# Optimization experiments

Hardware: AMD Instinct MI355X
Metric: run time of the kernel (lower is better)

The kernel has to match this reference:

```python
import jax, jax.numpy as jnp
import numpy as np


def _nn_mean_sqdist(source, target):
    # source: [N,3], target: [M,3]
    s_norm = jnp.sum(source ** 2, axis=1, keepdims=True)          # [N,1]
    t_norm = jnp.sum(target ** 2, axis=1, keepdims=True)          # [M,1]
    dist = s_norm + t_norm.T - 2.0 * (source @ target.T)          # [N,M] squared dists
    return jnp.min(dist, axis=1).mean()


def setup_inputs() -> dict:
    key = jax.random.key(0)
    k1, k2 = jax.random.split(key)
    pred_positions = jax.random.normal(k1, (16384, 3), dtype=jnp.float32)
    target_positions = jax.random.normal(k2, (16384, 3), dtype=jnp.float32)
    return {"pred_positions": pred_positions, "target_positions": target_positions}


def reference(pred_positions, target_positions):
    d_pt = _nn_mean_sqdist(pred_positions, target_positions)
    d_tp = _nn_mean_sqdist(target_positions, pred_positions)  # use_bidirectional=True
    return (d_pt + d_tp) / 2.0
```

## Files before the change

### kernel.cpp

```cpp
#include <hip/hip_runtime.h>

#define TPB 256

typedef __attribute__((ext_vector_type(8))) short bf16x8;
typedef __attribute__((ext_vector_type(16))) float f32x16;

__device__ inline unsigned short f2bf(float f) {
    unsigned u = __float_as_uint(f);
    return (unsigned short)((u + 0x7FFFu + ((u >> 16) & 1u)) >> 16);
}
__device__ inline float bf2f(unsigned short h) {
    return __uint_as_float((unsigned)h << 16);
}
__device__ inline uint4 pack8(unsigned short s0, unsigned short s1,
                              unsigned short s2, unsigned short s3,
                              unsigned short s4, unsigned short s5,
                              unsigned short s6, unsigned short s7) {
    uint4 v;
    v.x = (unsigned)s0 | ((unsigned)s1 << 16);
    v.y = (unsigned)s2 | ((unsigned)s3 << 16);
    v.z = (unsigned)s4 | ((unsigned)s5 << 16);
    v.w = (unsigned)s6 | ((unsigned)s7 << 16);
    return v;
}
__device__ inline bf16x8 as_frag(uint4 v) {
    union { uint4 u; bf16x8 f; } c; c.u = v; return c.f;
}

__global__ __launch_bounds__(TPB) void prep_kernel(
        const float* __restrict__ a, const float* __restrict__ b,
        uint4* __restrict__ pAa, uint4* __restrict__ pBa,
        uint4* __restrict__ pAb, uint4* __restrict__ pBb,
        float* __restrict__ norms, unsigned* __restrict__ pmins,
        float* __restrict__ acc, unsigned* __restrict__ cnt, int n) {
    int idx = blockIdx.x * TPB + threadIdx.x;
    if (idx < 2 * n) {
        int isB = idx >= n;
        int i = isB ? idx - n : idx;
        const float* s = isB ? b : a;
        float x = s[3 * i], y = s[3 * i + 1], z = s[3 * i + 2];
        float w = x * x + y * y + z * z;
        norms[idx] = w;
        float ax = -2.0f * x, ay = -2.0f * y, az = -2.0f * z;
        unsigned short ahx = f2bf(ax), ahy = f2bf(ay), ahz = f2bf(az);
        unsigned short alx = f2bf(ax - bf2f(ahx));
        unsigned short aly = f2bf(ay - bf2f(ahy));
        unsigned short alz = f2bf(az - bf2f(ahz));
        unsigned short thx = f2bf(x), thy = f2bf(y), thz = f2bf(z);
        unsigned short tlx = f2bf(x - bf2f(thx));
        unsigned short tly = f2bf(y - bf2f(thy));
        unsigned short tlz = f2bf(z - bf2f(thz));
        unsigned short wh = f2bf(w);  float r1 = w - bf2f(wh);
        unsigned short wm = f2bf(r1); float r2 = r1 - bf2f(wm);
        unsigned short wl = f2bf(r2);
        const unsigned short ONE = 0x3F80;
        uint4* Ad = (isB ? pAb : pAa) + (size_t)i * 2;
        uint4* Bd = (isB ? pBb : pBa) + (size_t)i * 2;
        Ad[0] = pack8(ahx, ahy, ahz, alx, aly, alz, ahx, ahy);
        Ad[1] = pack8(ahz, ONE, ONE, ONE, alx, aly, alz, 0);
        Bd[0] = pack8(thx, thy, thz, thx, thy, thz, tlx, tly);
        Bd[1] = pack8(tlz, wh, wm, wl, tlx, tly, tlz, 0);
        pmins[idx] = 0xFFFFFFFFu;
    }
    if (idx == 0) { acc[0] = 0.0f; cnt[0] = 0u; }
}

#define COMPUTE_TILE(X) do {                                                   \
    bf16x8 bb = as_frag(X);                                                    \
    f32x16 d0 = __builtin_amdgcn_mfma_f32_32x32x16_bf16(a0, bb, z, 0, 0, 0);   \
    f32x16 d1 = __builtin_amdgcn_mfma_f32_32x32x16_bf16(a1, bb, z, 0, 0, 0);   \
    _Pragma("unroll")                                                          \
    for (int i = 0; i < 16; ++i) {                                             \
        rm0[i] = fminf(rm0[i], d0[i]);                                         \
        rm1[i] = fminf(rm1[i], d1[i]);                                         \
    }                                                                          \
} while (0)

__global__ __launch_bounds__(TPB, 4) void minpass_kernel(
        const uint4* __restrict__ pAa, const uint4* __restrict__ pBa,
        const uint4* __restrict__ pAb, const uint4* __restrict__ pBb,
        const float* __restrict__ norms, unsigned* __restrict__ pmins, int n) {
    const int TS = 8;
    const int NRB = n / 256;
    const int TGT = n / TS;
    const int NT = TGT / 32;

    int bid = blockIdx.x;
    int dir = bid / (NRB * TS);
    int rem = bid % (NRB * TS);
    int rbk = rem / TS;
    int ts  = rem % TS;

    const uint4* __restrict__ Ap = dir ? pAb : pAa;
    const uint4* __restrict__ Bp = dir ? pBa : pBb;

    const int tid = threadIdx.x;
    const int wid = tid >> 6, lane = tid & 63;
    const int lr = lane & 31, lh = lane >> 5;

    const int rowbase = rbk * 256 + wid * 64;
    bf16x8 a0 = as_frag(Ap[(size_t)(rowbase + lr) * 2 + lh]);
    bf16x8 a1 = as_frag(Ap[(size_t)(rowbase + 32 + lr) * 2 + lh]);

    float rm0[16], rm1[16];
#pragma unroll
    for (int i = 0; i < 16; ++i) { rm0[i] = __builtin_inff(); rm1[i] = __builtin_inff(); }
    f32x16 z = {};

    const uint4* __restrict__ bp = Bp + (size_t)(ts * TGT + lr) * 2 + lh;

    uint4 A0 = bp[0], A1 = bp[64], A2 = bp[128], A3 = bp[192];
    for (int t = 0; t < NT - 4; t += 4) {
        COMPUTE_TILE(A0); A0 = bp[(t + 4) * 64];
        COMPUTE_TILE(A1); A1 = bp[(t + 5) * 64];
        COMPUTE_TILE(A2); A2 = bp[(t + 6) * 64];
        COMPUTE_TILE(A3); A3 = bp[(t + 7) * 64];
    }
    COMPUTE_TILE(A0); COMPUTE_TILE(A1); COMPUTE_TILE(A2); COMPUTE_TILE(A3);

#pragma unroll
    for (int k = 1; k < 32; k <<= 1) {
#pragma unroll
        for (int i = 0; i < 16; ++i) {
            rm0[i] = fminf(rm0[i], __shfl_xor(rm0[i], k, 64));
            rm1[i] = fminf(rm1[i], __shfl_xor(rm1[i], k, 64));
        }
    }
    if (lr == 0) {
        unsigned* pm = pmins + (size_t)dir * n;
        const float* nb = norms + (dir ? n : 0);
        int rb0 = rowbase + lh * 4;
#pragma unroll
        for (int i = 0; i < 16; ++i) {
            int r = (i & 3) + ((i >> 2) << 3);
            int r0 = rb0 + r, r1 = rb0 + 32 + r;
            atomicMin(&pm[r0], __float_as_uint(rm0[i] + nb[r0]));
            atomicMin(&pm[r1], __float_as_uint(rm1[i] + nb[r1]));
        }
    }
}

__global__ __launch_bounds__(TPB) void finalize_kernel(
        const uint4* __restrict__ pmins, float* __restrict__ acc,
        unsigned* __restrict__ cnt, float* __restrict__ out, int n, int nblocks) {
    int i = blockIdx.x * TPB + threadIdx.x;
    uint4 v = pmins[i];
    float sum = __uint_as_float(v.x) + __uint_as_float(v.y)
              + __uint_as_float(v.z) + __uint_as_float(v.w);
    for (int off = 32; off > 0; off >>= 1)
        sum += __shfl_down(sum, off, 64);
    __shared__ float wsum[TPB / 64];
    int lane = threadIdx.x & 63, wid = threadIdx.x >> 6;
    if (lane == 0) wsum[wid] = sum;
    __syncthreads();
    if (threadIdx.x == 0) {
        float t = 0.0f;
        for (int w = 0; w < TPB / 64; ++w) t += wsum[w];
        atomicAdd(acc, t);
        __threadfence();
        unsigned old = atomicAdd(cnt, 1u);
        if (old == (unsigned)(nblocks - 1)) {
            float a0 = atomicAdd(acc, 0.0f);
            out[0] = a0 / (float)(2 * n);
        }
    }
}

extern "C" void kernel_launch(void* const* d_in, const int* in_sizes, int n_in,
                              void* d_out, int out_size, void* d_ws, size_t ws_size,
                              hipStream_t stream) {
    const float* a = (const float*)d_in[0];
    const float* b = (const float*)d_in[1];
    int n = in_sizes[0] / 3;
    float* out = (float*)d_out;
    char* ws = (char*)d_ws;
    float* acc = (float*)ws;
    unsigned* cnt = (unsigned*)(ws + 8);
    float* norms = (float*)(ws + 256);
    char* packs = ws + 256 + (size_t)2 * n * 4;
    size_t psz = (size_t)n * 32;
    uint4* pAa = (uint4*)(packs);
    uint4* pBa = (uint4*)(packs + psz);
    uint4* pAb = (uint4*)(packs + 2 * psz);
    uint4* pBb = (uint4*)(packs + 3 * psz);
    unsigned* pmins = (unsigned*)(packs + 4 * psz);

    prep_kernel<<<(2 * n + TPB - 1) / TPB, TPB, 0, stream>>>(
        a, b, pAa, pBa, pAb, pBb, norms, pmins, acc, cnt, n);
    int mblocks = 2 * (n / 256) * 8;
    minpass_kernel<<<mblocks, TPB, 0, stream>>>(
        pAa, pBa, pAb, pBb, norms, pmins, n);
    int fblocks = (2 * n / 4) / TPB;
    finalize_kernel<<<fblocks, TPB, 0, stream>>>(
        (const uint4*)pmins, acc, cnt, out, n, fblocks);
}
```

Before: 85.64 us.

## Stage target tile in LDS and double the target split count

Each block now cooperatively copies its slice of packed target fragments into shared memory, then streams MFMA B operands from LDS instead of from global memory with register prefetch. The target dimension split goes from 8 to 16, so each block handles 1024 targets and the grid doubles. The aim is to cut the global/L2 load latency in the inner loop and add parallelism. The cost is more blocks, twice as many atomicMin writes, a 33KB LDS footprint that may limit occupancy, and a read one tile past the end into the padded buffer.

After: 93.87 us. 1.1x slower.

```diff
diff --git a/kernel.cpp b/kernel.cpp
--- a/kernel.cpp
+++ b/kernel.cpp
@@ -65,22 +65,11 @@
     if (idx == 0) { acc[0] = 0.0f; cnt[0] = 0u; }
 }
 
-#define COMPUTE_TILE(X) do {                                                   \
-    bf16x8 bb = as_frag(X);                                                    \
-    f32x16 d0 = __builtin_amdgcn_mfma_f32_32x32x16_bf16(a0, bb, z, 0, 0, 0);   \
-    f32x16 d1 = __builtin_amdgcn_mfma_f32_32x32x16_bf16(a1, bb, z, 0, 0, 0);   \
-    _Pragma("unroll")                                                          \
-    for (int i = 0; i < 16; ++i) {                                             \
-        rm0[i] = fminf(rm0[i], d0[i]);                                         \
-        rm1[i] = fminf(rm1[i], d1[i]);                                         \
-    }                                                                          \
-} while (0)
-
 __global__ __launch_bounds__(TPB, 4) void minpass_kernel(
         const uint4* __restrict__ pAa, const uint4* __restrict__ pBa,
         const uint4* __restrict__ pAb, const uint4* __restrict__ pBb,
         const float* __restrict__ norms, unsigned* __restrict__ pmins, int n) {
-    const int TS = 8;
+    const int TS = 16;
     const int NRB = n / 256;
     const int TGT = n / TS;
     const int NT = TGT / 32;
@@ -94,10 +83,19 @@
     const uint4* __restrict__ Ap = dir ? pAb : pAa;
     const uint4* __restrict__ Bp = dir ? pBa : pBb;
 
+    __shared__ uint4 sbuf[2048 + 64];
+
     const int tid = threadIdx.x;
     const int wid = tid >> 6, lane = tid & 63;
     const int lr = lane & 31, lh = lane >> 5;
 
+    {
+        const uint4* __restrict__ gs = Bp + (size_t)ts * TGT * 2;
+#pragma unroll
+        for (int i = 0; i < 8; ++i)
+            sbuf[tid + i * TPB] = gs[tid + i * TPB];
+    }
+
     const int rowbase = rbk * 256 + wid * 64;
     bf16x8 a0 = as_frag(Ap[(size_t)(rowbase + lr) * 2 + lh]);
     bf16x8 a1 = as_frag(Ap[(size_t)(rowbase + 32 + lr) * 2 + lh]);
@@ -107,16 +105,34 @@
     for (int i = 0; i < 16; ++i) { rm0[i] = __builtin_inff(); rm1[i] = __builtin_inff(); }
     f32x16 z = {};
 
-    const uint4* __restrict__ bp = Bp + (size_t)(ts * TGT + lr) * 2 + lh;
-
-    uint4 A0 = bp[0], A1 = bp[64], A2 = bp[128], A3 = bp[192];
-    for (int t = 0; t < NT - 4; t += 4) {
-        COMPUTE_TILE(A0); A0 = bp[(t + 4) * 64];
-        COMPUTE_TILE(A1); A1 = bp[(t + 5) * 64];
-        COMPUTE_TILE(A2); A2 = bp[(t + 6) * 64];
-        COMPUTE_TILE(A3); A3 = bp[(t + 7) * 64];
-    }
-    COMPUTE_TILE(A0); COMPUTE_TILE(A1); COMPUTE_TILE(A2); COMPUTE_TILE(A3);
+    __syncthreads();
+
+    const uint4* __restrict__ sb = sbuf + ((lr << 1) | lh);
+
+    bf16x8 b0 = as_frag(sb[0]);
+    for (int t = 0; t < NT; t += 2) {
+        bf16x8 b1 = as_frag(sb[(t + 1) * 64]);
+        {
+            f32x16 d0 = __builtin_amdgcn_mfma_f32_32x32x16_bf16(a0, b0, z, 0, 0, 0);
+            f32x16 d1 = __builtin_amdgcn_mfma_f32_32x32x16_bf16(a1, b0, z, 0, 0, 0);
+#pragma unroll
+            for (int i = 0; i < 16; ++i) {
+                rm0[i] = fminf(rm0[i], d0[i]);
+                rm1[i] = fminf(rm1[i], d1[i]);
+            }
+        }
+        bf16x8 b2 = as_frag(sb[(t + 2) * 64]);
+        {
+            f32x16 d0 = __builtin_amdgcn_mfma_f32_32x32x16_bf16(a0, b1, z, 0, 0, 0);
+            f32x16 d1 = __builtin_amdgcn_mfma_f32_32x32x16_bf16(a1, b1, z, 0, 0, 0);
+#pragma unroll
+            for (int i = 0; i < 16; ++i) {
+                rm0[i] = fminf(rm0[i], d0[i]);
+                rm1[i] = fminf(rm1[i], d1[i]);
+            }
+        }
+        b0 = b2;
+    }
 
 #pragma unroll
     for (int k = 1; k < 32; k <<= 1) {
@@ -187,7 +203,7 @@
 
     prep_kernel<<<(2 * n + TPB - 1) / TPB, TPB, 0, stream>>>(
         a, b, pAa, pBa, pAb, pBb, norms, pmins, acc, cnt, n);
-    int mblocks = 2 * (n / 256) * 8;
+    int mblocks = 2 * (n / 256) * 16;
     minpass_kernel<<<mblocks, TPB, 0, stream>>>(
         pAa, pBa, pAb, pBb, norms, pmins, n);
     int fblocks = (2 * n / 4) / TPB;
```

## Compute both directions from one distance matrix using row and column minima

Applied to the files above, without the earlier changes.

Instead of computing the N×M distance matrix twice (once per direction), the kernel computes the full squared distance (both norms folded into the MFMA operands) once and takes row minima via registers/atomics and column minima via LDS atomicMin per tile. Per-block column minima are written to a workspace and reduced across 64 row blocks in the finalize kernel. This halves the MFMA work but adds per-tile column reductions, LDS atomics, a large intermediate buffer and lowers occupancy to 2 blocks per SIMD group.

Result: no change. 85.58 us (-0.1%).

```diff
diff --git a/kernel.cpp b/kernel.cpp
--- a/kernel.cpp
+++ b/kernel.cpp
@@ -29,23 +29,29 @@
 
 __global__ __launch_bounds__(TPB) void prep_kernel(
         const float* __restrict__ a, const float* __restrict__ b,
-        uint4* __restrict__ pAa, uint4* __restrict__ pBa,
-        uint4* __restrict__ pAb, uint4* __restrict__ pBb,
-        float* __restrict__ norms, unsigned* __restrict__ pmins,
+        uint4* __restrict__ pA, uint4* __restrict__ pB,
+        unsigned* __restrict__ pmins,
         float* __restrict__ acc, unsigned* __restrict__ cnt, int n) {
     int idx = blockIdx.x * TPB + threadIdx.x;
-    if (idx < 2 * n) {
-        int isB = idx >= n;
-        int i = isB ? idx - n : idx;
-        const float* s = isB ? b : a;
-        float x = s[3 * i], y = s[3 * i + 1], z = s[3 * i + 2];
+    const unsigned short ONE = 0x3F80;
+    if (idx < n) {
+        float x = a[3 * idx], y = a[3 * idx + 1], z = a[3 * idx + 2];
         float w = x * x + y * y + z * z;
-        norms[idx] = w;
         float ax = -2.0f * x, ay = -2.0f * y, az = -2.0f * z;
         unsigned short ahx = f2bf(ax), ahy = f2bf(ay), ahz = f2bf(az);
         unsigned short alx = f2bf(ax - bf2f(ahx));
         unsigned short aly = f2bf(ay - bf2f(ahy));
         unsigned short alz = f2bf(az - bf2f(ahz));
+        unsigned short wh = f2bf(w);  float r1 = w - bf2f(wh);
+        unsigned short wm = f2bf(r1); float r2 = r1 - bf2f(wm);
+        unsigned short wl = f2bf(r2);
+        pA[(size_t)idx * 2 + 0] = pack8(ahx, ahy, ahz, alx, aly, alz, ahx, ahy);
+        pA[(size_t)idx * 2 + 1] = pack8(ahz, wh, wm, wl, ONE, ONE, ONE, 0);
+        pmins[idx] = 0xFFFFFFFFu;
+    } else if (idx < 2 * n) {
+        int i = idx - n;
+        float x = b[3 * i], y = b[3 * i + 1], z = b[3 * i + 2];
+        float w = x * x + y * y + z * z;
         unsigned short thx = f2bf(x), thy = f2bf(y), thz = f2bf(z);
         unsigned short tlx = f2bf(x - bf2f(thx));
         unsigned short tly = f2bf(y - bf2f(thy));
@@ -53,19 +59,46 @@
         unsigned short wh = f2bf(w);  float r1 = w - bf2f(wh);
         unsigned short wm = f2bf(r1); float r2 = r1 - bf2f(wm);
         unsigned short wl = f2bf(r2);
-        const unsigned short ONE = 0x3F80;
-        uint4* Ad = (isB ? pAb : pAa) + (size_t)i * 2;
-        uint4* Bd = (isB ? pBb : pBa) + (size_t)i * 2;
-        Ad[0] = pack8(ahx, ahy, ahz, alx, aly, alz, ahx, ahy);
-        Ad[1] = pack8(ahz, ONE, ONE, ONE, alx, aly, alz, 0);
-        Bd[0] = pack8(thx, thy, thz, thx, thy, thz, tlx, tly);
-        Bd[1] = pack8(tlz, wh, wm, wl, tlx, tly, tlz, 0);
-        pmins[idx] = 0xFFFFFFFFu;
+        pB[(size_t)i * 2 + 0] = pack8(thx, thy, thz, thx, thy, thz, tlx, tly);
+        pB[(size_t)i * 2 + 1] = pack8(tlz, ONE, ONE, ONE, wh, wm, wl, 0);
     }
     if (idx == 0) { acc[0] = 0.0f; cnt[0] = 0u; }
 }
 
-#define COMPUTE_TILE(X) do {                                                   \
+__global__ __launch_bounds__(TPB, 2) void minpass_kernel(
+        const uint4* __restrict__ pA, const uint4* __restrict__ pB,
+        unsigned* __restrict__ pmins, unsigned* __restrict__ cm_out, int n) {
+    const int TS = 8;
+    const int NRB = n / 256;
+    const int TGT = n / TS;
+    const int NT = TGT / 32;
+
+    int bid = blockIdx.x;
+    int rbk = bid % NRB;
+    int ts  = bid / NRB;
+
+    __shared__ unsigned cm[2048];
+
+    const int tid = threadIdx.x;
+    for (int i = tid; i < TGT; i += TPB) cm[i] = 0xFFFFFFFFu;
+
+    const int wid = tid >> 6, lane = tid & 63;
+    const int lr = lane & 31, lh = lane >> 5;
+
+    const int rowbase = rbk * 256 + wid * 64;
+    bf16x8 a0 = as_frag(pA[(size_t)(rowbase + lr) * 2 + lh]);
+    bf16x8 a1 = as_frag(pA[(size_t)(rowbase + 32 + lr) * 2 + lh]);
+
+    float rm0[16], rm1[16];
+#pragma unroll
+    for (int i = 0; i < 16; ++i) { rm0[i] = __builtin_inff(); rm1[i] = __builtin_inff(); }
+    f32x16 z = {};
+
+    const uint4* __restrict__ bp = pB + (size_t)(ts * TGT + lr) * 2 + lh;
+
+    __syncthreads();
+
+#define TILE(X, T) do {                                                        \
     bf16x8 bb = as_frag(X);                                                    \
     f32x16 d0 = __builtin_amdgcn_mfma_f32_32x32x16_bf16(a0, bb, z, 0, 0, 0);   \
     f32x16 d1 = __builtin_amdgcn_mfma_f32_32x32x16_bf16(a1, bb, z, 0, 0, 0);   \
@@ -74,49 +107,27 @@
         rm0[i] = fminf(rm0[i], d0[i]);                                         \
         rm1[i] = fminf(rm1[i], d1[i]);                                         \
     }                                                                          \
+    float t8[8];                                                               \
+    _Pragma("unroll")                                                          \
+    for (int i = 0; i < 8; ++i)                                                \
+        t8[i] = fminf(fminf(d0[i], d0[i + 8]), fminf(d1[i], d1[i + 8]));       \
+    float c0 = fminf(fminf(t8[0], t8[1]), t8[2]);                              \
+    float c1 = fminf(fminf(t8[3], t8[4]), t8[5]);                              \
+    float c2 = fminf(t8[6], t8[7]);                                            \
+    float cmin = fminf(fminf(c0, c1), c2);                                     \
+    atomicMin(&cm[(T) * 32 + lr], __float_as_uint(cmin));                      \
 } while (0)
 
-__global__ __launch_bounds__(TPB, 4) void minpass_kernel(
-        const uint4* __restrict__ pAa, const uint4* __restrict__ pBa,
-        const uint4* __restrict__ pAb, const uint4* __restrict__ pBb,
-        const float* __restrict__ norms, unsigned* __restrict__ pmins, int n) {
-    const int TS = 8;
-    const int NRB = n / 256;
-    const int TGT = n / TS;
-    const int NT = TGT / 32;
-
-    int bid = blockIdx.x;
-    int dir = bid / (NRB * TS);
-    int rem = bid % (NRB * TS);
-    int rbk = rem / TS;
-    int ts  = rem % TS;
-
-    const uint4* __restrict__ Ap = dir ? pAb : pAa;
-    const uint4* __restrict__ Bp = dir ? pBa : pBb;
-
-    const int tid = threadIdx.x;
-    const int wid = tid >> 6, lane = tid & 63;
-    const int lr = lane & 31, lh = lane >> 5;
-
-    const int rowbase = rbk * 256 + wid * 64;
-    bf16x8 a0 = as_frag(Ap[(size_t)(rowbase + lr) * 2 + lh]);
-    bf16x8 a1 = as_frag(Ap[(size_t)(rowbase + 32 + lr) * 2 + lh]);
-
-    float rm0[16], rm1[16];
-#pragma unroll
-    for (int i = 0; i < 16; ++i) { rm0[i] = __builtin_inff(); rm1[i] = __builtin_inff(); }
-    f32x16 z = {};
-
-    const uint4* __restrict__ bp = Bp + (size_t)(ts * TGT + lr) * 2 + lh;
-
-    uint4 A0 = bp[0], A1 = bp[64], A2 = bp[128], A3 = bp[192];
-    for (int t = 0; t < NT - 4; t += 4) {
-        COMPUTE_TILE(A0); A0 = bp[(t + 4) * 64];
-        COMPUTE_TILE(A1); A1 = bp[(t + 5) * 64];
-        COMPUTE_TILE(A2); A2 = bp[(t + 6) * 64];
-        COMPUTE_TILE(A3); A3 = bp[(t + 7) * 64];
-    }
-    COMPUTE_TILE(A0); COMPUTE_TILE(A1); COMPUTE_TILE(A2); COMPUTE_TILE(A3);
+    uint4 P0 = bp[0], P1 = bp[64], P2 = bp[128], P3 = bp[192];
+    int t = 0;
+    for (; t + 4 < NT; t += 4) {
+        TILE(P0, t);     P0 = bp[(t + 4) * 64];
+        TILE(P1, t + 1); P1 = bp[(t + 5) * 64];
+        TILE(P2, t + 2); P2 = bp[(t + 6) * 64];
+        TILE(P3, t + 3); P3 = bp[(t + 7) * 64];
+    }
+    TILE(P0, t); TILE(P1, t + 1); TILE(P2, t + 2); TILE(P3, t + 3);
+#undef TILE
 
 #pragma unroll
     for (int k = 1; k < 32; k <<= 1) {
@@ -127,26 +138,45 @@
         }
     }
     if (lr == 0) {
-        unsigned* pm = pmins + (size_t)dir * n;
-        const float* nb = norms + (dir ? n : 0);
         int rb0 = rowbase + lh * 4;
 #pragma unroll
         for (int i = 0; i < 16; ++i) {
             int r = (i & 3) + ((i >> 2) << 3);
-            int r0 = rb0 + r, r1 = rb0 + 32 + r;
-            atomicMin(&pm[r0], __float_as_uint(rm0[i] + nb[r0]));
-            atomicMin(&pm[r1], __float_as_uint(rm1[i] + nb[r1]));
-        }
+            atomicMin(&pmins[rb0 + r], __float_as_uint(rm0[i]));
+            atomicMin(&pmins[rb0 + 32 + r], __float_as_uint(rm1[i]));
+        }
+    }
+
+    __syncthreads();
+    {
+        unsigned* __restrict__ co = cm_out + (size_t)rbk * n + ts * TGT;
+        for (int i = tid; i < TGT; i += TPB) co[i] = cm[i];
     }
 }
 
 __global__ __launch_bounds__(TPB) void finalize_kernel(
-        const uint4* __restrict__ pmins, float* __restrict__ acc,
-        unsigned* __restrict__ cnt, float* __restrict__ out, int n, int nblocks) {
-    int i = blockIdx.x * TPB + threadIdx.x;
-    uint4 v = pmins[i];
-    float sum = __uint_as_float(v.x) + __uint_as_float(v.y)
-              + __uint_as_float(v.z) + __uint_as_float(v.w);
+        const uint4* __restrict__ pmins4, const uint4* __restrict__ cm4,
+        float* __restrict__ acc, unsigned* __restrict__ cnt,
+        float* __restrict__ out, int n, int nblocks) {
+    int b = blockIdx.x;
+    float sum;
+    if (b < 16) {
+        uint4 v = pmins4[b * TPB + threadIdx.x];
+        sum = __uint_as_float(v.x) + __uint_as_float(v.y)
+            + __uint_as_float(v.z) + __uint_as_float(v.w);
+    } else {
+        int c4 = (b - 16) * TPB + threadIdx.x;
+        const int stride = n / 4;
+        uint4 m = cm4[c4];
+#pragma unroll
+        for (int r = 1; r < 64; ++r) {
+            uint4 v = cm4[(size_t)r * stride + c4];
+            m.x = min(m.x, v.x); m.y = min(m.y, v.y);
+            m.z = min(m.z, v.z); m.w = min(m.w, v.w);
+        }
+        sum = __uint_as_float(m.x) + __uint_as_float(m.y)
+            + __uint_as_float(m.z) + __uint_as_float(m.w);
+    }
     for (int off = 32; off > 0; off >>= 1)
         sum += __shfl_down(sum, off, 64);
     __shared__ float wsum[TPB / 64];
@@ -154,9 +184,9 @@
     if (lane == 0) wsum[wid] = sum;
     __syncthreads();
     if (threadIdx.x == 0) {
-        float t = 0.0f;
-        for (int w = 0; w < TPB / 64; ++w) t += wsum[w];
-        atomicAdd(acc, t);
+        float tsum = 0.0f;
+        for (int w = 0; w < TPB / 64; ++w) tsum += wsum[w];
+        atomicAdd(acc, tsum);
         __threadfence();
         unsigned old = atomicAdd(cnt, 1u);
         if (old == (unsigned)(nblocks - 1)) {
@@ -176,21 +206,16 @@
     char* ws = (char*)d_ws;
     float* acc = (float*)ws;
     unsigned* cnt = (unsigned*)(ws + 8);
-    float* norms = (float*)(ws + 256);
-    char* packs = ws + 256 + (size_t)2 * n * 4;
-    size_t psz = (size_t)n * 32;
-    uint4* pAa = (uint4*)(packs);
-    uint4* pBa = (uint4*)(packs + psz);
-    uint4* pAb = (uint4*)(packs + 2 * psz);
-    uint4* pBb = (uint4*)(packs + 3 * psz);
-    unsigned* pmins = (unsigned*)(packs + 4 * psz);
+    uint4* pA = (uint4*)(ws + 256);
+    uint4* pB = (uint4*)(ws + 256 + (size_t)n * 32);
+    unsigned* cm_out = (unsigned*)(ws + 256 + (size_t)n * 64);
+    unsigned* pmins = (unsigned*)(ws + 256 + (size_t)n * 64
+                                  + (size_t)(n / 256) * n * 4);
 
     prep_kernel<<<(2 * n + TPB - 1) / TPB, TPB, 0, stream>>>(
-        a, b, pAa, pBa, pAb, pBb, norms, pmins, acc, cnt, n);
-    int mblocks = 2 * (n / 256) * 8;
-    minpass_kernel<<<mblocks, TPB, 0, stream>>>(
-        pAa, pBa, pAb, pBb, norms, pmins, n);
-    int fblocks = (2 * n / 4) / TPB;
-    finalize_kernel<<<fblocks, TPB, 0, stream>>>(
-        (const uint4*)pmins, acc, cnt, out, n, fblocks);
-}
+        a, b, pA, pB, pmins, acc, cnt, n);
+    int mblocks = (n / 256) * 8;
+    minpass_kernel<<<mblocks, TPB, 0, stream>>>(pA, pB, pmins, cm_out, n);
+    finalize_kernel<<<32, TPB, 0, stream>>>(
+        (const uint4*)pmins, (const uint4*)cm_out, acc, cnt, out, n, 32);
+}
```
